# Performance work log

Measured on AMD Instinct MI355X. Metric: run time of the kernel, lower is better.

The kernel has to match this reference:

```python
import jax, jax.numpy as jnp
import numpy as np

N_NODES = 100000
N_EDGES = 1600000
IN_CH = 256
HID_CH = 256
OUT_CH = 40


def gcn_conv(x, W, b, src, dst, n):
    """PyG GCNConv with default symmetric normalization and self-loops,
    edge_weight = 1. out_i = sum_{j->i} d_i^{-1/2} d_j^{-1/2} (x_j W) + d_i^{-1} (x_i W) + b
    where d includes the self-loop (+1)."""
    h = x @ W  # [n, out]
    deg = jnp.zeros((n,), x.dtype).at[dst].add(1.0) + 1.0  # +1 self-loop
    dinv = jax.lax.rsqrt(deg)
    norm = dinv[src] * dinv[dst]                      # [E]
    msg = h[src] * norm[:, None]                      # [E, out] gather
    agg = jnp.zeros_like(h).at[dst].add(msg)          # scatter-add
    agg = agg + h * (dinv * dinv)[:, None]            # self-loop term
    return agg + b


def setup_inputs() -> dict:
    key = jax.random.key(0)
    ks = jax.random.split(key, 8)
    x = jax.random.normal(ks[0], (N_NODES, IN_CH), jnp.float32)
    edge_index = jax.random.randint(ks[1], (2, N_EDGES), 0, N_NODES, jnp.int64)
    s1 = 1.0 / np.sqrt(IN_CH)
    s2 = 1.0 / np.sqrt(HID_CH)
    W1 = jax.random.normal(ks[2], (IN_CH, HID_CH), jnp.float32) * s1
    b1 = jnp.zeros((HID_CH,), jnp.float32)
    W2 = jax.random.normal(ks[3], (HID_CH, HID_CH), jnp.float32) * s2
    b2 = jnp.zeros((HID_CH,), jnp.float32)
    W3 = jax.random.normal(ks[4], (HID_CH, OUT_CH), jnp.float32) * s2
    b3 = jnp.zeros((OUT_CH,), jnp.float32)
    return {"x": x, "edge_index": edge_index, "W1": W1, "b1": b1,
            "W2": W2, "b2": b2, "W3": W3, "b3": b3}


def reference(x, edge_index, W1, b1, W2, b2, W3, b3):
    src, dst = edge_index[0], edge_index[1]
    n = x.shape[0]
    # layer 1: conv -> relu (batch_norm=False, dropout inactive in eval)
    h = jax.nn.relu(gcn_conv(x, W1, b1, src, dst, n))
    # layer 2
    h = jax.nn.relu(gcn_conv(h, W2, b2, src, dst, n))
    # final layer + log_softmax
    h = gcn_conv(h, W3, b3, src, dst, n)
    return jax.nn.log_softmax(h, axis=-1)
```

## Files before the change

### kernel.cpp

```cpp
#include <hip/hip_runtime.h>
#include <math.h>
#include <cstddef>

#define NN 100000
#define NE 1600000
#define CH 256
#define OC 40

typedef __attribute__((ext_vector_type(8))) short bf16x8;
typedef __attribute__((ext_vector_type(4))) float f32x4;

static __device__ __forceinline__ unsigned short f2bf(float f) {
    unsigned int u = __float_as_uint(f);
    unsigned int r = (u + 0x7FFFu + ((u >> 16) & 1u)) >> 16;
    return (unsigned short)r;
}
static __device__ __forceinline__ float bflo(unsigned int u) {
    return __uint_as_float(u << 16);
}
static __device__ __forceinline__ float bfhi(unsigned int u) {
    return __uint_as_float(u & 0xFFFF0000u);
}


__global__ void hist_kernel(const int* __restrict__ dst, int* __restrict__ deg, int E) {
    int i = blockIdx.x * blockDim.x + threadIdx.x;
    int st = gridDim.x * blockDim.x;
    for (; i < E; i += st) atomicAdd(&deg[dst[i]], 1);
}

__global__ void dinv_kernel(const int* __restrict__ deg, float* __restrict__ dinv, int n) {
    int i = blockIdx.x * blockDim.x + threadIdx.x;
    if (i < n) dinv[i] = rsqrtf((float)deg[i] + 1.0f);
}

__global__ __launch_bounds__(256) void scan1_kernel(const int* __restrict__ deg,
        int* __restrict__ row_ptr, int* __restrict__ bsum, int n) {
    __shared__ int s[256];
    int t = threadIdx.x;
    int i = blockIdx.x * 256 + t;
    int v = (i < n) ? deg[i] + 1 : 0;
    s[t] = v;
    __syncthreads();
    #pragma unroll
    for (int off = 1; off < 256; off <<= 1) {
        int u = (t >= off) ? s[t - off] : 0;
        __syncthreads();
        s[t] += u;
        __syncthreads();
    }
    if (i < n) row_ptr[i] = s[t] - v;
    if (t == 255) bsum[blockIdx.x] = s[255];
}

__global__ __launch_bounds__(512) void scan2_kernel(const int* __restrict__ bsum,
        int* __restrict__ boff, int* __restrict__ row_ptr, int nb, int n) {
    __shared__ int s[512];
    int t = threadIdx.x;
    int v = (t < nb) ? bsum[t] : 0;
    s[t] = v;
    __syncthreads();
    #pragma unroll
    for (int off = 1; off < 512; off <<= 1) {
        int u = (t >= off) ? s[t - off] : 0;
        __syncthreads();
        s[t] += u;
        __syncthreads();
    }
    if (t < nb) boff[t] = s[t] - v;
    if (t == nb - 1) row_ptr[n] = s[t];
}

__global__ __launch_bounds__(256) void scan3_kernel(int* __restrict__ row_ptr,
        const int* __restrict__ boff, int n) {
    int i = blockIdx.x * 256 + threadIdx.x;
    if (i < n) row_ptr[i] += boff[i >> 8];
}

__global__ void fill_kernel(const int* __restrict__ src, const int* __restrict__ dst,
                            const int* __restrict__ row_ptr, int* __restrict__ cursor,
                            const float* __restrict__ dinv,
                            int* __restrict__ csr_src, float* __restrict__ csr_norm,
                            int E, int n) {
    int i = blockIdx.x * blockDim.x + threadIdx.x;
    int st = gridDim.x * blockDim.x;
    int total = E + n;
    for (; i < total; i += st) {
        if (i < E) {
            int s = src[i], d = dst[i];
            int pos = row_ptr[d] + atomicAdd(&cursor[d], 1);
            csr_src[pos] = s;
            csr_norm[pos] = dinv[s] * dinv[d];
        } else {
            int v = i - E;
            int pos = row_ptr[v + 1] - 1;
            csr_src[pos] = v;
            csr_norm[pos] = dinv[v] * dinv[v];
        }
    }
}


__global__ void f2b8_kernel(const float* __restrict__ in, unsigned short* __restrict__ out,
                            int ngroups) {
    int i = blockIdx.x * blockDim.x + threadIdx.x;
    if (i >= ngroups) return;
    float4 a = reinterpret_cast<const float4*>(in)[(size_t)i * 2];
    float4 b = reinterpret_cast<const float4*>(in)[(size_t)i * 2 + 1];
    uint4 r;
    r.x = f2bf(a.x) | ((unsigned)f2bf(a.y) << 16);
    r.y = f2bf(a.z) | ((unsigned)f2bf(a.w) << 16);
    r.z = f2bf(b.x) | ((unsigned)f2bf(b.y) << 16);
    r.w = f2bf(b.z) | ((unsigned)f2bf(b.w) << 16);
    reinterpret_cast<uint4*>(out)[i] = r;
}

__global__ void wtrans_kernel(const float* __restrict__ W, unsigned short* __restrict__ Wt) {
    __shared__ float tile[16][17];
    int k = blockIdx.y * 16 + threadIdx.y;
    int n = blockIdx.x * 16 + threadIdx.x;
    tile[threadIdx.y][threadIdx.x] = W[(size_t)k * 256 + n];
    __syncthreads();
    int on = blockIdx.x * 16 + threadIdx.y;
    int ok = blockIdx.y * 16 + threadIdx.x;
    Wt[(size_t)on * 256 + ok] = f2bf(tile[threadIdx.x][threadIdx.y]);
}

__global__ __launch_bounds__(256) void gemm_bf16_kernel(
        const unsigned short* __restrict__ A, const unsigned short* __restrict__ Wt,
        unsigned short* __restrict__ C, int M) {
    __shared__ __align__(16) unsigned short As[128 * 40];
    __shared__ __align__(16) unsigned short Bs[128 * 40];
    const int t = threadIdx.x;
    const int l = t & 63;
    const int w = t >> 6;
    const int wr = w >> 1, wc = w & 1;
    const int row0 = blockIdx.x * 128;
    const int col0 = blockIdx.y * 128;

    f32x4 acc[4][4];
    #pragma unroll
    for (int m = 0; m < 4; m++)
        #pragma unroll
        for (int n = 0; n < 4; n++) acc[m][n] = (f32x4){0.f, 0.f, 0.f, 0.f};

    const int sr = t >> 2;
    const int sc = (t & 3) * 8;
    const int rl = l & 15;
    const int kb = (l >> 4) * 8;

    uint4 va[2], ub[2];
    #pragma unroll
    for (int p = 0; p < 2; p++) {
        int r = sr + p * 64;
        int gr = row0 + r;
        va[p] = (gr < M) ? *reinterpret_cast<const uint4*>(A + (size_t)gr * 256 + sc)
                         : make_uint4(0u, 0u, 0u, 0u);
        ub[p] = *reinterpret_cast<const uint4*>(Wt + (size_t)(col0 + r) * 256 + sc);
    }

    for (int k0 = 0; k0 < 256; k0 += 32) {
        #pragma unroll
        for (int p = 0; p < 2; p++) {
            int r = sr + p * 64;
            *reinterpret_cast<uint4*>(&As[r * 40 + sc]) = va[p];
            *reinterpret_cast<uint4*>(&Bs[r * 40 + sc]) = ub[p];
        }
        __syncthreads();
        if (k0 + 32 < 256) {
            #pragma unroll
            for (int p = 0; p < 2; p++) {
                int r = sr + p * 64;
                int gr = row0 + r;
                va[p] = (gr < M) ? *reinterpret_cast<const uint4*>(A + (size_t)gr * 256 + k0 + 32 + sc)
                                 : make_uint4(0u, 0u, 0u, 0u);
                ub[p] = *reinterpret_cast<const uint4*>(Wt + (size_t)(col0 + r) * 256 + k0 + 32 + sc);
            }
        }
        bf16x8 af[4], bfr[4];
        #pragma unroll
        for (int m = 0; m < 4; m++)
            af[m] = *reinterpret_cast<const bf16x8*>(&As[(wr * 64 + m * 16 + rl) * 40 + kb]);
        #pragma unroll
        for (int n = 0; n < 4; n++)
            bfr[n] = *reinterpret_cast<const bf16x8*>(&Bs[(wc * 64 + n * 16 + rl) * 40 + kb]);
        #pragma unroll
        for (int m = 0; m < 4; m++)
            #pragma unroll
            for (int n = 0; n < 4; n++)
                acc[m][n] = __builtin_amdgcn_mfma_f32_16x16x32_bf16(af[m], bfr[n], acc[m][n], 0, 0, 0);
        __syncthreads();
    }
    const int rh = l >> 4;
    #pragma unroll
    for (int m = 0; m < 4; m++) {
        #pragma unroll
        for (int n = 0; n < 4; n++) {
            #pragma unroll
            for (int j = 0; j < 4; j++) {
                int gr = row0 + wr * 64 + m * 16 + rh * 4 + j;
                int gc = col0 + wc * 64 + n * 16 + rl;
                if (gr < M) C[(size_t)gr * 256 + gc] = f2bf(acc[m][n][j]);
            }
        }
    }
}

__global__ __launch_bounds__(256) void gemm40_kernel(const unsigned short* __restrict__ A,
                                                     const float* __restrict__ W,
                                                     float* __restrict__ C, int M) {
    __shared__ float Hs[128][65];
    __shared__ float Ws[64][40];
    const int t = threadIdx.x;
    const int tr = t & 127;
    const int tg = t >> 7;
    const int row0 = blockIdx.x * 128;
    float acc[20];
    #pragma unroll
    for (int j = 0; j < 20; j++) acc[j] = 0.f;

    const int hr = t >> 4;
    const int hc = (t & 15) << 2;

    for (int k0 = 0; k0 < 256; k0 += 64) {
        #pragma unroll
        for (int p = 0; p < 8; p++) {
            int r = hr + p * 16;
            int gr = row0 + r;
            uint2 u = make_uint2(0u, 0u);
            if (gr < M) u = *reinterpret_cast<const uint2*>(A + (size_t)gr * 256 + k0 + hc);
            Hs[r][hc] = bflo(u.x); Hs[r][hc + 1] = bfhi(u.x);
            Hs[r][hc + 2] = bflo(u.y); Hs[r][hc + 3] = bfhi(u.y);
        }
        for (int i = t; i < 64 * 40; i += 256) {
            int r = i / 40, c = i - r * 40;
            Ws[r][c] = W[(size_t)(k0 + r) * 40 + c];
        }
        __syncthreads();
        #pragma unroll 4
        for (int kk = 0; kk < 64; ++kk) {
            float a = Hs[tr][kk];
            float b[20];
            #pragma unroll
            for (int q = 0; q < 5; q++)
                *reinterpret_cast<float4*>(&b[q * 4]) =
                    *reinterpret_cast<float4*>(&Ws[kk][tg * 20 + q * 4]);
            #pragma unroll
            for (int j = 0; j < 20; j++) acc[j] = fmaf(a, b[j], acc[j]);
        }
        __syncthreads();
    }
    int gr = row0 + tr;
    if (gr < M) {
        #pragma unroll
        for (int q = 0; q < 5; q++) {
            float4 v = make_float4(acc[q * 4], acc[q * 4 + 1], acc[q * 4 + 2], acc[q * 4 + 3]);
            *reinterpret_cast<float4*>(C + (size_t)gr * 40 + tg * 20 + q * 4) = v;
        }
    }
}

__global__ __launch_bounds__(256) void aggb_kernel(const unsigned short* __restrict__ T,
        const int* __restrict__ row_ptr, const int* __restrict__ csr_src,
        const float* __restrict__ csr_norm, const float* __restrict__ bias,
        unsigned short* __restrict__ H, int n, int do_relu) {
    int wid = threadIdx.x >> 6, lane = threadIdx.x & 63;
    int node = blockIdx.x * 4 + wid;
    if (node >= n) return;
    int e0 = row_ptr[node], end = row_ptr[node + 1];
    float a0 = 0.f, a1 = 0.f, a2 = 0.f, a3 = 0.f;
    for (int base = e0; base < end; base += 64) {
        int cnt = min(64, end - base);
        int sv = 0; float wv = 0.f;
        if (lane < cnt) { sv = csr_src[base + lane]; wv = csr_norm[base + lane]; }
        int j = 0;
        for (; j + 3 < cnt; j += 4) {
            int s0 = __shfl(sv, j),     s1 = __shfl(sv, j + 1);
            int s2 = __shfl(sv, j + 2), s3 = __shfl(sv, j + 3);
            float w0 = __shfl(wv, j),     w1 = __shfl(wv, j + 1);
            float w2 = __shfl(wv, j + 2), w3 = __shfl(wv, j + 3);
            uint2 u0 = *reinterpret_cast<const uint2*>(T + (size_t)s0 * 256 + lane * 4);
            uint2 u1 = *reinterpret_cast<const uint2*>(T + (size_t)s1 * 256 + lane * 4);
            uint2 u2 = *reinterpret_cast<const uint2*>(T + (size_t)s2 * 256 + lane * 4);
            uint2 u3 = *reinterpret_cast<const uint2*>(T + (size_t)s3 * 256 + lane * 4);
            a0 = fmaf(w0, bflo(u0.x), a0); a1 = fmaf(w0, bfhi(u0.x), a1);
            a2 = fmaf(w0, bflo(u0.y), a2); a3 = fmaf(w0, bfhi(u0.y), a3);
            a0 = fmaf(w1, bflo(u1.x), a0); a1 = fmaf(w1, bfhi(u1.x), a1);
            a2 = fmaf(w1, bflo(u1.y), a2); a3 = fmaf(w1, bfhi(u1.y), a3);
            a0 = fmaf(w2, bflo(u2.x), a0); a1 = fmaf(w2, bfhi(u2.x), a1);
            a2 = fmaf(w2, bflo(u2.y), a2); a3 = fmaf(w2, bfhi(u2.y), a3);
            a0 = fmaf(w3, bflo(u3.x), a0); a1 = fmaf(w3, bfhi(u3.x), a1);
            a2 = fmaf(w3, bflo(u3.y), a2); a3 = fmaf(w3, bfhi(u3.y), a3);
        }
        for (; j < cnt; ++j) {
            int s0 = __shfl(sv, j);
            float w0 = __shfl(wv, j);
            uint2 u0 = *reinterpret_cast<const uint2*>(T + (size_t)s0 * 256 + lane * 4);
            a0 = fmaf(w0, bflo(u0.x), a0); a1 = fmaf(w0, bfhi(u0.x), a1);
            a2 = fmaf(w0, bflo(u0.y), a2); a3 = fmaf(w0, bfhi(u0.y), a3);
        }
    }
    float4 bb = reinterpret_cast<const float4*>(bias)[lane];
    a0 += bb.x; a1 += bb.y; a2 += bb.z; a3 += bb.w;
    if (do_relu) {
        a0 = fmaxf(a0, 0.f); a1 = fmaxf(a1, 0.f);
        a2 = fmaxf(a2, 0.f); a3 = fmaxf(a3, 0.f);
    }
    uint2 o;
    o.x = f2bf(a0) | ((unsigned)f2bf(a1) << 16);
    o.y = f2bf(a2) | ((unsigned)f2bf(a3) << 16);
    *reinterpret_cast<uint2*>(H + (size_t)node * 256 + lane * 4) = o;
}

__global__ __launch_bounds__(256) void agg40_kernel(const float* __restrict__ T3,
        const int* __restrict__ row_ptr, const int* __restrict__ csr_src,
        const float* __restrict__ csr_norm, const float* __restrict__ bias,
        float* __restrict__ Out, int n) {
    int wid = threadIdx.x >> 6, lane = threadIdx.x & 63;
    int node = blockIdx.x * 4 + wid;
    if (node >= n) return;
    bool act = lane < OC;
    int e0 = row_ptr[node], end = row_ptr[node + 1];
    float acc = 0.f;
    for (int base = e0; base < end; base += 64) {
        int cnt = min(64, end - base);
        int sv = 0; float wv = 0.f;
        if (lane < cnt) { sv = csr_src[base + lane]; wv = csr_norm[base + lane]; }
        int j = 0;
        for (; j + 3 < cnt; j += 4) {
            int s0 = __shfl(sv, j),     s1 = __shfl(sv, j + 1);
            int s2 = __shfl(sv, j + 2), s3 = __shfl(sv, j + 3);
            float w0 = __shfl(wv, j),     w1 = __shfl(wv, j + 1);
            float w2 = __shfl(wv, j + 2), w3 = __shfl(wv, j + 3);
            float v0 = act ? T3[(size_t)s0 * OC + lane] : 0.f;
            float v1 = act ? T3[(size_t)s1 * OC + lane] : 0.f;
            float v2 = act ? T3[(size_t)s2 * OC + lane] : 0.f;
            float v3 = act ? T3[(size_t)s3 * OC + lane] : 0.f;
            acc = fmaf(w0, v0, acc);
            acc = fmaf(w1, v1, acc);
            acc = fmaf(w2, v2, acc);
            acc = fmaf(w3, v3, acc);
        }
        for (; j < cnt; ++j) {
            int s0 = __shfl(sv, j);
            float w0 = __shfl(wv, j);
            float v0 = act ? T3[(size_t)s0 * OC + lane] : 0.f;
            acc = fmaf(w0, v0, acc);
        }
    }
    float bb = act ? bias[lane] : 0.f;
    float x = act ? (acc + bb) : -INFINITY;
    float m = x;
    #pragma unroll
    for (int off = 32; off; off >>= 1) m = fmaxf(m, __shfl_xor(m, off));
    float ex = act ? expf(x - m) : 0.f;
    float ssum = ex;
    #pragma unroll
    for (int off = 32; off; off >>= 1) ssum += __shfl_xor(ssum, off);
    if (act) Out[(size_t)node * OC + lane] = x - m - logf(ssum);
}


extern "C" void kernel_launch(void* const* d_in, const int* in_sizes, int n_in,
                              void* d_out, int out_size, void* d_ws, size_t ws_size,
                              hipStream_t stream) {
    const float* x  = (const float*)d_in[0];
    const int* ei   = (const int*)d_in[1];
    const int* esrc = ei;
    const int* edst = ei + NE;
    const float* W1 = (const float*)d_in[2];
    const float* b1 = (const float*)d_in[3];
    const float* W2 = (const float*)d_in[4];
    const float* b2 = (const float*)d_in[5];
    const float* W3 = (const float*)d_in[6];
    const float* b3 = (const float*)d_in[7];
    float* out = (float*)d_out;

    char* p = (char*)d_ws;
    int* deg      = (int*)p;   p += 400000;
    int* cursor   = (int*)p;   p += 400000;
    int* row_ptr  = (int*)p;   p += 400128;
    float* dinv   = (float*)p; p += 400000;
    int* bsum     = (int*)p;   p += 2048;
    int* boff     = (int*)p;   p += 2048;
    int* csr_src  = (int*)p;   p += (size_t)(NE + NN) * 4;
    float* csr_nm = (float*)p; p += (size_t)(NE + NN) * 4;
    unsigned short* Xb  = (unsigned short*)p; p += (size_t)NN * CH * 2;
    unsigned short* Wt1 = (unsigned short*)p; p += 256 * 256 * 2;
    unsigned short* Wt2 = (unsigned short*)p; p += 256 * 256 * 2;
    unsigned short* Tb  = (unsigned short*)p; p += (size_t)NN * CH * 2;
    unsigned short* Hb  = (unsigned short*)p; p += (size_t)NN * CH * 2;
    float* T3     = (float*)p; p += (size_t)NN * OC * 4;

    hipMemsetAsync(deg, 0, 800000, stream);

    const int nb = (NN + 255) / 256;

    hist_kernel<<<2048, 256, 0, stream>>>(edst, deg, NE);
    dinv_kernel<<<(NN + 255) / 256, 256, 0, stream>>>(deg, dinv, NN);
    scan1_kernel<<<nb, 256, 0, stream>>>(deg, row_ptr, bsum, NN);
    scan2_kernel<<<1, 512, 0, stream>>>(bsum, boff, NN ? row_ptr : row_ptr, nb, NN);
    scan3_kernel<<<nb, 256, 0, stream>>>(row_ptr, boff, NN);
    fill_kernel<<<2048, 256, 0, stream>>>(esrc, edst, row_ptr, cursor, dinv,
                                          csr_src, csr_nm, NE, NN);

    f2b8_kernel<<<(NN * CH / 8 + 255) / 256, 256, 0, stream>>>(x, Xb, NN * CH / 8);
    {
        dim3 g(16, 16), b(16, 16);
        wtrans_kernel<<<g, b, 0, stream>>>(W1, Wt1);
        wtrans_kernel<<<g, b, 0, stream>>>(W2, Wt2);
    }

    dim3 gg((NN + 127) / 128, 2);
    gemm_bf16_kernel<<<gg, 256, 0, stream>>>(Xb, Wt1, Tb, NN);
    aggb_kernel<<<NN / 4, 256, 0, stream>>>(Tb, row_ptr, csr_src, csr_nm, b1, Hb, NN, 1);
    gemm_bf16_kernel<<<gg, 256, 0, stream>>>(Hb, Wt2, Tb, NN);
    aggb_kernel<<<NN / 4, 256, 0, stream>>>(Tb, row_ptr, csr_src, csr_nm, b2, Hb, NN, 1);
    gemm40_kernel<<<(NN + 127) / 128, 256, 0, stream>>>(Hb, W3, T3, NN);
    agg40_kernel<<<NN / 4, 256, 0, stream>>>(T3, row_ptr, csr_src, csr_nm, b3, out, NN);
}
```

Measured before the change: 855.8 us.

## Fuse fp32-to-bf16 conversion into layer-1 GEMM and drop per-edge norm array

Layer 1's GEMM now reads fp32 x directly and converts to bf16 while staging tiles, so the separate conversion pass and its bf16 copy of x go away. The per-edge normalization array is removed: aggregation kernels look up dinv of each source on the fly and scale by the destination's dinv once at the end. The fill kernel writes only source indices, and the cursor is seeded from row_ptr by a small copy kernel. This trades an extra dependent gather (dinv[src]) per edge in every aggregation for less memory traffic in the preprocessing stage.

```diff
diff --git a/kernel.cpp b/kernel.cpp
--- a/kernel.cpp
+++ b/kernel.cpp
@@ -20,6 +20,16 @@
 }
 static __device__ __forceinline__ float bfhi(unsigned int u) {
     return __uint_as_float(u & 0xFFFF0000u);
+}
+static __device__ __forceinline__ uint4 ld_f32x8_to_bf8(const float* p) {
+    float4 a = *reinterpret_cast<const float4*>(p);
+    float4 b = *reinterpret_cast<const float4*>(p + 4);
+    uint4 r;
+    r.x = f2bf(a.x) | ((unsigned)f2bf(a.y) << 16);
+    r.y = f2bf(a.z) | ((unsigned)f2bf(a.w) << 16);
+    r.z = f2bf(b.x) | ((unsigned)f2bf(b.y) << 16);
+    r.w = f2bf(b.z) | ((unsigned)f2bf(b.w) << 16);
+    return r;
 }
 
 
@@ -77,43 +87,30 @@
     if (i < n) row_ptr[i] += boff[i >> 8];
 }
 
+__global__ __launch_bounds__(256) void cpy_kernel(const int* __restrict__ rp,
+        int* __restrict__ cursor, int n) {
+    int i = blockIdx.x * 256 + threadIdx.x;
+    if (i < n) cursor[i] = rp[i];
+}
+
 __global__ void fill_kernel(const int* __restrict__ src, const int* __restrict__ dst,
                             const int* __restrict__ row_ptr, int* __restrict__ cursor,
-                            const float* __restrict__ dinv,
-                            int* __restrict__ csr_src, float* __restrict__ csr_norm,
-                            int E, int n) {
+                            int* __restrict__ csr_src, int E, int n) {
     int i = blockIdx.x * blockDim.x + threadIdx.x;
     int st = gridDim.x * blockDim.x;
     int total = E + n;
     for (; i < total; i += st) {
         if (i < E) {
             int s = src[i], d = dst[i];
-            int pos = row_ptr[d] + atomicAdd(&cursor[d], 1);
+            int pos = atomicAdd(&cursor[d], 1);
             csr_src[pos] = s;
-            csr_norm[pos] = dinv[s] * dinv[d];
         } else {
             int v = i - E;
-            int pos = row_ptr[v + 1] - 1;
-            csr_src[pos] = v;
-            csr_norm[pos] = dinv[v] * dinv[v];
-        }
-    }
-}
-
-
-__global__ void f2b8_kernel(const float* __restrict__ in, unsigned short* __restrict__ out,
-                            int ngroups) {
-    int i = blockIdx.x * blockDim.x + threadIdx.x;
-    if (i >= ngroups) return;
-    float4 a = reinterpret_cast<const float4*>(in)[(size_t)i * 2];
-    float4 b = reinterpret_cast<const float4*>(in)[(size_t)i * 2 + 1];
-    uint4 r;
-    r.x = f2bf(a.x) | ((unsigned)f2bf(a.y) << 16);
-    r.y = f2bf(a.z) | ((unsigned)f2bf(a.w) << 16);
-    r.z = f2bf(b.x) | ((unsigned)f2bf(b.y) << 16);
-    r.w = f2bf(b.z) | ((unsigned)f2bf(b.w) << 16);
-    reinterpret_cast<uint4*>(out)[i] = r;
-}
+            csr_src[row_ptr[v + 1] - 1] = v;
+        }
+    }
+}
+
 
 __global__ void wtrans_kernel(const float* __restrict__ W, unsigned short* __restrict__ Wt) {
     __shared__ float tile[16][17];
@@ -124,6 +121,86 @@
     int on = blockIdx.x * 16 + threadIdx.y;
     int ok = blockIdx.y * 16 + threadIdx.x;
     Wt[(size_t)on * 256 + ok] = f2bf(tile[threadIdx.x][threadIdx.y]);
+}
+
+__global__ __launch_bounds__(256) void gemm_l1_kernel(
+        const float* __restrict__ A, const unsigned short* __restrict__ Wt,
+        unsigned short* __restrict__ C, int M) {
+    __shared__ __align__(16) unsigned short As[128 * 40];
+    __shared__ __align__(16) unsigned short Bs[128 * 40];
+    const int t = threadIdx.x;
+    const int l = t & 63;
+    const int w = t >> 6;
+    const int wr = w >> 1, wc = w & 1;
+    const int row0 = blockIdx.x * 128;
+    const int col0 = blockIdx.y * 128;
+
+    f32x4 acc[4][4];
+    #pragma unroll
+    for (int m = 0; m < 4; m++)
+        #pragma unroll
+        for (int n = 0; n < 4; n++) acc[m][n] = (f32x4){0.f, 0.f, 0.f, 0.f};
+
+    const int sr = t >> 2;
+    const int sc = (t & 3) * 8;
+    const int rl = l & 15;
+    const int kb = (l >> 4) * 8;
+
+    uint4 va[2], ub[2];
+    #pragma unroll
+    for (int p = 0; p < 2; p++) {
+        int r = sr + p * 64;
+        int gr = row0 + r;
+        va[p] = (gr < M) ? ld_f32x8_to_bf8(A + (size_t)gr * 256 + sc)
+                         : make_uint4(0u, 0u, 0u, 0u);
+        ub[p] = *reinterpret_cast<const uint4*>(Wt + (size_t)(col0 + r) * 256 + sc);
+    }
+
+    for (int k0 = 0; k0 < 256; k0 += 32) {
+        #pragma unroll
+        for (int p = 0; p < 2; p++) {
+            int r = sr + p * 64;
+            *reinterpret_cast<uint4*>(&As[r * 40 + sc]) = va[p];
+            *reinterpret_cast<uint4*>(&Bs[r * 40 + sc]) = ub[p];
+        }
+        __syncthreads();
+        if (k0 + 32 < 256) {
+            #pragma unroll
+            for (int p = 0; p < 2; p++) {
+                int r = sr + p * 64;
+                int gr = row0 + r;
+                va[p] = (gr < M) ? ld_f32x8_to_bf8(A + (size_t)gr * 256 + k0 + 32 + sc)
+                                 : make_uint4(0u, 0u, 0u, 0u);
+                ub[p] = *reinterpret_cast<const uint4*>(Wt + (size_t)(col0 + r) * 256 + k0 + 32 + sc);
+            }
+        }
+        bf16x8 af[4], bfr[4];
+        #pragma unroll
+        for (int m = 0; m < 4; m++)
+            af[m] = *reinterpret_cast<const bf16x8*>(&As[(wr * 64 + m * 16 + rl) * 40 + kb]);
+        #pragma unroll
+        for (int n = 0; n < 4; n++)
+            bfr[n] = *reinterpret_cast<const bf16x8*>(&Bs[(wc * 64 + n * 16 + rl) * 40 + kb]);
+        #pragma unroll
+        for (int m = 0; m < 4; m++)
+            #pragma unroll
+            for (int n = 0; n < 4; n++)
+                acc[m][n] = __builtin_amdgcn_mfma_f32_16x16x32_bf16(af[m], bfr[n], acc[m][n], 0, 0, 0);
+        __syncthreads();
+    }
+    const int rh = l >> 4;
+    #pragma unroll
+    for (int m = 0; m < 4; m++) {
+        #pragma unroll
+        for (int n = 0; n < 4; n++) {
+            #pragma unroll
+            for (int j = 0; j < 4; j++) {
+                int gr = row0 + wr * 64 + m * 16 + rh * 4 + j;
+                int gc = col0 + wc * 64 + n * 16 + rl;
+                if (gr < M) C[(size_t)gr * 256 + gc] = f2bf(acc[m][n][j]);
+            }
+        }
+    }
 }
 
 __global__ __launch_bounds__(256) void gemm_bf16_kernel(
@@ -262,17 +339,18 @@
 
 __global__ __launch_bounds__(256) void aggb_kernel(const unsigned short* __restrict__ T,
         const int* __restrict__ row_ptr, const int* __restrict__ csr_src,
-        const float* __restrict__ csr_norm, const float* __restrict__ bias,
+        const float* __restrict__ dinv, const float* __restrict__ bias,
         unsigned short* __restrict__ H, int n, int do_relu) {
     int wid = threadIdx.x >> 6, lane = threadIdx.x & 63;
     int node = blockIdx.x * 4 + wid;
     if (node >= n) return;
     int e0 = row_ptr[node], end = row_ptr[node + 1];
+    float dn = dinv[node];
     float a0 = 0.f, a1 = 0.f, a2 = 0.f, a3 = 0.f;
     for (int base = e0; base < end; base += 64) {
         int cnt = min(64, end - base);
         int sv = 0; float wv = 0.f;
-        if (lane < cnt) { sv = csr_src[base + lane]; wv = csr_norm[base + lane]; }
+        if (lane < cnt) { sv = csr_src[base + lane]; wv = dinv[sv]; }
         int j = 0;
         for (; j + 3 < cnt; j += 4) {
             int s0 = __shfl(sv, j),     s1 = __shfl(sv, j + 1);
@@ -301,7 +379,8 @@
         }
     }
     float4 bb = reinterpret_cast<const float4*>(bias)[lane];
-    a0 += bb.x; a1 += bb.y; a2 += bb.z; a3 += bb.w;
+    a0 = fmaf(a0, dn, bb.x); a1 = fmaf(a1, dn, bb.y);
+    a2 = fmaf(a2, dn, bb.z); a3 = fmaf(a3, dn, bb.w);
     if (do_relu) {
         a0 = fmaxf(a0, 0.f); a1 = fmaxf(a1, 0.f);
         a2 = fmaxf(a2, 0.f); a3 = fmaxf(a3, 0.f);
@@ -314,18 +393,19 @@
 
 __global__ __launch_bounds__(256) void agg40_kernel(const float* __restrict__ T3,
         const int* __restrict__ row_ptr, const int* __restrict__ csr_src,
-        const float* __restrict__ csr_norm, const float* __restrict__ bias,
+        const float* __restrict__ dinv, const float* __restrict__ bias,
         float* __restrict__ Out, int n) {
     int wid = threadIdx.x >> 6, lane = threadIdx.x & 63;
     int node = blockIdx.x * 4 + wid;
     if (node >= n) return;
     bool act = lane < OC;
     int e0 = row_ptr[node], end = row_ptr[node + 1];
+    float dn = dinv[node];
     float acc = 0.f;
     for (int base = e0; base < end; base += 64) {
         int cnt = min(64, end - base);
         int sv = 0; float wv = 0.f;
-        if (lane < cnt) { sv = csr_src[base + lane]; wv = csr_norm[base + lane]; }
+        if (lane < cnt) { sv = csr_src[base + lane]; wv = dinv[sv]; }
         int j = 0;
         for (; j + 3 < cnt; j += 4) {
             int s0 = __shfl(sv, j),     s1 = __shfl(sv, j + 1);
@@ -349,7 +429,7 @@
         }
     }
     float bb = act ? bias[lane] : 0.f;
-    float x = act ? (acc + bb) : -INFINITY;
+    float x = act ? (acc * dn + bb) : -INFINITY;
     float m = x;
     #pragma unroll
     for (int off = 32; off; off >>= 1) m = fmaxf(m, __shfl_xor(m, off));
@@ -384,27 +464,24 @@
     int* bsum     = (int*)p;   p += 2048;
     int* boff     = (int*)p;   p += 2048;
     int* csr_src  = (int*)p;   p += (size_t)(NE + NN) * 4;
-    float* csr_nm = (float*)p; p += (size_t)(NE + NN) * 4;
-    unsigned short* Xb  = (unsigned short*)p; p += (size_t)NN * CH * 2;
     unsigned short* Wt1 = (unsigned short*)p; p += 256 * 256 * 2;
     unsigned short* Wt2 = (unsigned short*)p; p += 256 * 256 * 2;
     unsigned short* Tb  = (unsigned short*)p; p += (size_t)NN * CH * 2;
     unsigned short* Hb  = (unsigned short*)p; p += (size_t)NN * CH * 2;
     float* T3     = (float*)p; p += (size_t)NN * OC * 4;
 
-    hipMemsetAsync(deg, 0, 800000, stream);
+    hipMemsetAsync(deg, 0, 400000, stream);
 
     const int nb = (NN + 255) / 256;
 
     hist_kernel<<<2048, 256, 0, stream>>>(edst, deg, NE);
-    dinv_kernel<<<(NN + 255) / 256, 256, 0, stream>>>(deg, dinv, NN);
+    dinv_kernel<<<nb, 256, 0, stream>>>(deg, dinv, NN);
     scan1_kernel<<<nb, 256, 0, stream>>>(deg, row_ptr, bsum, NN);
-    scan2_kernel<<<1, 512, 0, stream>>>(bsum, boff, NN ? row_ptr : row_ptr, nb, NN);
+    scan2_kernel<<<1, 512, 0, stream>>>(bsum, boff, row_ptr, nb, NN);
     scan3_kernel<<<nb, 256, 0, stream>>>(row_ptr, boff, NN);
-    fill_kernel<<<2048, 256, 0, stream>>>(esrc, edst, row_ptr, cursor, dinv,
-                                          csr_src, csr_nm, NE, NN);
-
-    f2b8_kernel<<<(NN * CH / 8 + 255) / 256, 256, 0, stream>>>(x, Xb, NN * CH / 8);
+    cpy_kernel<<<nb, 256, 0, stream>>>(row_ptr, cursor, NN);
+    fill_kernel<<<2048, 256, 0, stream>>>(esrc, edst, row_ptr, cursor, csr_src, NE, NN);
+
     {
         dim3 g(16, 16), b(16, 16);
         wtrans_kernel<<<g, b, 0, stream>>>(W1, Wt1);
@@ -412,10 +489,10 @@
     }
 
     dim3 gg((NN + 127) / 128, 2);
-    gemm_bf16_kernel<<<gg, 256, 0, stream>>>(Xb, Wt1, Tb, NN);
-    aggb_kernel<<<NN / 4, 256, 0, stream>>>(Tb, row_ptr, csr_src, csr_nm, b1, Hb, NN, 1);
+    gemm_l1_kernel<<<gg, 256, 0, stream>>>(x, Wt1, Tb, NN);
+    aggb_kernel<<<NN / 4, 256, 0, stream>>>(Tb, row_ptr, csr_src, dinv, b1, Hb, NN, 1);
     gemm_bf16_kernel<<<gg, 256, 0, stream>>>(Hb, Wt2, Tb, NN);
-    aggb_kernel<<<NN / 4, 256, 0, stream>>>(Tb, row_ptr, csr_src, csr_nm, b2, Hb, NN, 1);
+    aggb_kernel<<<NN / 4, 256, 0, stream>>>(Tb, row_ptr, csr_src, dinv, b2, Hb, NN, 1);
     gemm40_kernel<<<(NN + 127) / 128, 256, 0, stream>>>(Hb, W3, T3, NN);
-    agg40_kernel<<<NN / 4, 256, 0, stream>>>(T3, row_ptr, csr_src, csr_nm, b3, out, NN);
-}
+    agg40_kernel<<<NN / 4, 256, 0, stream>>>(T3, row_ptr, csr_src, dinv, b3, out, NN);
+}
```

After: 864.0 us. No clear change (+1.0%).
